# Performance work log

Hardware: AMD Instinct MI355X
Metric: run time of the kernel (lower is better)

The kernel has to match this reference:

```python
import jax, jax.numpy as jnp
import numpy as np

N = 100000
E = 1000000
IN_DIM = 64
ATT_DIM = 32


def setup_inputs() -> dict:
    key = jax.random.key(0)
    ks = jax.random.split(key, 9)
    x = jax.random.normal(ks[0], (N, IN_DIM), dtype=jnp.float32)
    src1 = jax.random.randint(ks[1], (E,), 0, N, dtype=jnp.int32)
    dst1 = jax.random.randint(ks[2], (E,), 0, N, dtype=jnp.int32)
    src2 = jax.random.randint(ks[3], (E,), 0, N, dtype=jnp.int32)
    dst2 = jax.random.randint(ks[4], (E,), 0, N, dtype=jnp.int32)
    # Learned params: w_o (in_dim -> att_dim), att (att_dim -> 1)
    W_o = jax.random.normal(ks[5], (IN_DIM, ATT_DIM), dtype=jnp.float32) / np.sqrt(IN_DIM)
    b_o = jnp.zeros((ATT_DIM,), dtype=jnp.float32)
    W_att = jax.random.normal(ks[6], (ATT_DIM, 1), dtype=jnp.float32) / np.sqrt(ATT_DIM)
    b_att = jnp.zeros((1,), dtype=jnp.float32)
    return {"x": x, "W_o": W_o, "b_o": b_o, "W_att": W_att, "b_att": b_att,
            "src1": src1, "dst1": dst1, "src2": src2, "dst2": dst2}


def _edge_softmax_agg(h, a, src, dst):
    """edge_softmax of source logits grouped by dst, then weighted sum of src feats."""
    a_e = a[src]  # [E] per-edge logit copied from source node (copy_u)
    m = jax.ops.segment_max(a_e, dst, num_segments=N)  # per-dst max for stability
    m = jnp.where(jnp.isfinite(m), m, 0.0)
    e = jnp.exp(a_e - jax.lax.stop_gradient(m)[dst])
    s = jax.ops.segment_sum(e, dst, num_segments=N)  # per-dst normalizer
    w = e / s[dst]  # normalized edge attention [E]
    # u_mul_e + sum reduction
    return jax.ops.segment_sum(h[src] * w[:, None], dst, num_segments=N)  # [N, in_dim]


def reference(x, W_o, b_o, W_att, b_att, src1, dst1, src2, dst2):
    # a = att(w_o(h))  (note: self.activation is defined but unused in forward)
    a = ((x @ W_o + b_o) @ W_att + b_att)[:, 0]  # [N]
    h1 = _edge_softmax_agg(x, a, src1, dst1)
    h2 = _edge_softmax_agg(x, a, src2, dst2)
    # multi_update_all cross-type 'mean' over the 2 edge types
    return (h1 + h2) * 0.5
```

## Files before the change

kernel.cpp:

```cpp
#include <hip/hip_runtime.h>
#include <hip/hip_bf16.h>

#define IN_DIM 64
#define BSHIFT 7
#define BSIZE  128
#define CHUNK  8192
#define PBLK   512
#define MAXNB1 1024
#define CAPMAX 1600
#define GBLK   256

__device__ __forceinline__ float bflo(unsigned int u) { return __uint_as_float(u << 16); }
__device__ __forceinline__ float bfhi(unsigned int u) { return __uint_as_float(u & 0xFFFF0000u); }
__device__ __forceinline__ unsigned short f2bf(float f) {
    __hip_bfloat16 b = __float2bfloat16(f);
    return *reinterpret_cast<unsigned short*>(&b);
}

#define ACC8(A, e, v)                        \
    A[0] = fmaf(e, bflo((v).x), A[0]);       \
    A[1] = fmaf(e, bfhi((v).x), A[1]);       \
    A[2] = fmaf(e, bflo((v).y), A[2]);       \
    A[3] = fmaf(e, bfhi((v).y), A[3]);       \
    A[4] = fmaf(e, bflo((v).z), A[4]);       \
    A[5] = fmaf(e, bfhi((v).z), A[5]);       \
    A[6] = fmaf(e, bflo((v).w), A[6]);       \
    A[7] = fmaf(e, bfhi((v).w), A[7]);

__global__ __launch_bounds__(PBLK) void logits_partition_kernel(
        const float* __restrict__ x,
        const float* __restrict__ W_o,
        const float* __restrict__ b_o,
        const float* __restrict__ W_att,
        const float* __restrict__ b_att,
        float* __restrict__ ea,
        unsigned short* __restrict__ xh, int N,
        const int* __restrict__ src1,
        const int* __restrict__ dst1,
        const int* __restrict__ src2,
        const int* __restrict__ dst2,
        int* __restrict__ gCtr,
        int* __restrict__ packed,
        int E, int NB1, int CAP, int chunks1) {
    __shared__ int spk[CHUNK];
    __shared__ unsigned short sbk[CHUNK];
    __shared__ int hist[MAXNB1];
    __shared__ int lbase[MAXNB1];
    __shared__ int gb2[MAXNB1];
    __shared__ int scr[PBLK];
    __shared__ float vsh[IN_DIM];
    __shared__ float csh;
    int pb = 2 * chunks1;
    int t = threadIdx.x;
    if (blockIdx.x < pb) {
        int b = blockIdx.x;
        int type = (b >= chunks1) ? 1 : 0;
        int ci = type ? (b - chunks1) : b;
        const int* src = type ? src2 : src1;
        const int* dst = type ? dst2 : dst1;
        int e0 = ci * CHUNK;
        int e1 = min(E, e0 + CHUNK);
        int cnt = e1 - e0;
        for (int i = t; i < MAXNB1; i += PBLK) hist[i] = 0;
        __syncthreads();
        for (int e = e0 + t; e < e1; e += PBLK)
            atomicAdd(&hist[dst[e] >> BSHIFT], 1);
        __syncthreads();
        int a0 = hist[2 * t], a1 = hist[2 * t + 1];
        int s = a0 + a1;
        scr[t] = s;
        __syncthreads();
        int val = s;
        for (int off = 1; off < PBLK; off <<= 1) {
            int u = (t >= off) ? scr[t - off] : 0;
            __syncthreads();
            val += u;
            scr[t] = val;
            __syncthreads();
        }
        int ex = val - s;
        lbase[2 * t] = ex;
        lbase[2 * t + 1] = ex + a0;
        __syncthreads();
        for (int i = t; i < NB1; i += PBLK) {
            int h = hist[i];
            gb2[i] = (h ? atomicAdd(&gCtr[type * NB1 + i], h) : 0) - lbase[i];
            hist[i] = lbase[i];
        }
        __syncthreads();
        for (int e = e0 + t; e < e1; e += PBLK) {
            int d = dst[e];
            int bk = d >> BSHIFT;
            int lrank = atomicAdd(&hist[bk], 1);
            spk[lrank] = src[e] | ((d & (BSIZE - 1)) << 17);
            sbk[lrank] = (unsigned short)bk;
        }
        __syncthreads();
        for (int i = t; i < cnt; i += PBLK) {
            int bk = sbk[i];
            int lrk = gb2[bk] + i;
            if (lrk < CAP)
                packed[(size_t)(type * NB1 + bk) * CAP + lrk] = spk[i];
        }
    } else {
        if (t < IN_DIM) {
            float acc = 0.f;
#pragma unroll
            for (int k = 0; k < 32; ++k) acc += W_o[t * 32 + k] * W_att[k];
            vsh[t] = acc;
        }
        if (t == IN_DIM) {
            float acc = b_att[0];
#pragma unroll
            for (int k = 0; k < 32; ++k) acc += b_o[k] * W_att[k];
            csh = acc;
        }
        __syncthreads();
        int node = (blockIdx.x - pb) * 32 + (t >> 4);
        int fq = t & 15;
        if (node >= N) return;
        const float4 xv = *(const float4*)(x + (size_t)node * 64 + fq * 4);
        ushort4 st;
        st.x = f2bf(xv.x); st.y = f2bf(xv.y); st.z = f2bf(xv.z); st.w = f2bf(xv.w);
        *(ushort4*)(xh + (size_t)node * 64 + fq * 4) = st;
        float val = xv.x * vsh[fq * 4 + 0] + xv.y * vsh[fq * 4 + 1] +
                    xv.z * vsh[fq * 4 + 2] + xv.w * vsh[fq * 4 + 3];
        val += __shfl_xor(val, 1);
        val += __shfl_xor(val, 2);
        val += __shfl_xor(val, 4);
        val += __shfl_xor(val, 8);
        if (fq == 0) ea[node] = expf(val + csh);
    }
}

__global__ __launch_bounds__(GBLK, 5) void csr_gather_kernel(
        const int* __restrict__ gCtr,
        const int* __restrict__ packed,
        const float* __restrict__ ea,
        const unsigned short* __restrict__ xh,
        float* __restrict__ out, int N, int NB1, int CAP) {
    __shared__ int2 pae[2][CAPMAX];
    __shared__ int  hist[2][BSIZE];
    __shared__ int  exv [2][BSIZE];
    __shared__ int  cur [BSIZE];
    int nb = blockIdx.x;
    int t = threadIdx.x;

#pragma unroll
    for (int type = 0; type < 2; ++type) {
        int r = type * NB1 + nb;
        int cnt = min(gCtr[r], CAP);
        const int* seg = packed + (size_t)r * CAP;
        if (t < BSIZE) hist[type][t] = 0;
        __syncthreads();
        for (int i = t; i < cnt; i += GBLK)
            atomicAdd(&hist[type][seg[i] >> 17], 1);
        __syncthreads();
        int v = 0, val = 0;
        if (t < BSIZE) { v = hist[type][t]; val = v; cur[t] = v; }
        __syncthreads();
        for (int off = 1; off < BSIZE; off <<= 1) {
            int u = 0;
            if (t < BSIZE && t >= off) u = cur[t - off];
            __syncthreads();
            if (t < BSIZE) { val += u; cur[t] = val; }
            __syncthreads();
        }
        if (t < BSIZE) { exv[type][t] = val - v; cur[t] = val - v; }
        __syncthreads();
        for (int i = t; i < cnt; i += GBLK) {
            int p = seg[i];
            int s = p & 0x1FFFF;
            int pos = atomicAdd(&cur[p >> 17], 1);
            pae[type][pos] = make_int2(s, __float_as_int(ea[s]));
        }
        __syncthreads();
    }

    int gid = t >> 3;
    int fl  = t & 7;
    const unsigned short* xrow = xh + (fl << 3);

    for (int ni = 0; ni < 4; ++ni) {
        int dl = (ni << 5) + gid;
        float rr[8] = {0,0,0,0,0,0,0,0};
#pragma unroll
        for (int type = 0; type < 2; ++type) {
            int k0 = exv[type][dl];
            int deg = hist[type][dl];
            if (deg <= 0) continue;
            float accP[8] = {0,0,0,0,0,0,0,0};
            float accQ[8] = {0,0,0,0,0,0,0,0};
            float ewP = 0.f, ewQ = 0.f;
            int h = deg >> 1;
            for (int j = 0; j < h; ++j) {
                int2 p1 = pae[type][k0 + j];
                int2 p2 = pae[type][k0 + h + j];
                const uint4 v1 = *(const uint4*)(xrow + (size_t)p1.x * 64);
                const uint4 v2 = *(const uint4*)(xrow + (size_t)p2.x * 64);
                float e1 = __int_as_float(p1.y);
                float e2 = __int_as_float(p2.y);
                ewP += e1; ewQ += e2;
                ACC8(accP, e1, v1);
                ACC8(accQ, e2, v2);
            }
            if (deg & 1) {
                int2 p1 = pae[type][k0 + deg - 1];
                const uint4 v1 = *(const uint4*)(xrow + (size_t)p1.x * 64);
                float e1 = __int_as_float(p1.y);
                ewP += e1;
                ACC8(accP, e1, v1);
            }
            float inv = 1.f / (ewP + ewQ);
#pragma unroll
            for (int k = 0; k < 8; ++k)
                rr[k] = fmaf(accP[k] + accQ[k], inv, rr[k]);
        }
        int node = (nb << BSHIFT) + dl;
        if (node < N) {
            float* op = out + (size_t)node * 64 + (fl << 3);
            *(float4*)op       = make_float4(0.5f * rr[0], 0.5f * rr[1], 0.5f * rr[2], 0.5f * rr[3]);
            *(float4*)(op + 4) = make_float4(0.5f * rr[4], 0.5f * rr[5], 0.5f * rr[6], 0.5f * rr[7]);
        }
    }
}

extern "C" void kernel_launch(void* const* d_in, const int* in_sizes, int n_in,
                              void* d_out, int out_size, void* d_ws, size_t ws_size,
                              hipStream_t stream) {
    const float* x     = (const float*)d_in[0];
    const float* W_o   = (const float*)d_in[1];
    const float* b_o   = (const float*)d_in[2];
    const float* W_att = (const float*)d_in[3];
    const float* b_att = (const float*)d_in[4];
    const int*   src1  = (const int*)d_in[5];
    const int*   dst1  = (const int*)d_in[6];
    const int*   src2  = (const int*)d_in[7];
    const int*   dst2  = (const int*)d_in[8];
    float* out = (float*)d_out;

    const int N = in_sizes[0] / IN_DIM;
    const int E = in_sizes[5];
    const int NB1 = (N + BSIZE - 1) >> BSHIFT;
    const int avg = (E + NB1 - 1) / NB1;
    int CAP = avg + avg / 6 + 32;
    if (CAP > CAPMAX) CAP = CAPMAX;

    char* wp = (char*)d_ws;
    auto take = [&](size_t bytes) { char* p = wp; wp += (bytes + 63) & ~63ull; return p; };
    float* ea          = (float*)take((size_t)N * 4);
    int* gCtr          = (int*)take((size_t)2 * NB1 * 4);
    unsigned short* xh = (unsigned short*)take((size_t)N * 64 * 2);
    int* packed        = (int*)take((size_t)2 * NB1 * CAP * 4);

    hipMemsetAsync(gCtr, 0, (size_t)2 * NB1 * sizeof(int), stream);

    int chunks1 = (E + CHUNK - 1) / CHUNK;
    int logitBlocks = (N + 31) / 32;
    logits_partition_kernel<<<2 * chunks1 + logitBlocks, PBLK, 0, stream>>>(
        x, W_o, b_o, W_att, b_att, ea, xh, N,
        src1, dst1, src2, dst2, gCtr, packed, E, NB1, CAP, chunks1);

    csr_gather_kernel<<<NB1, GBLK, 0, stream>>>(gCtr, packed, ea, xh, out,
                                                N, NB1, CAP);
}
```

Baseline: 80.60 us.

## Use wavefront shuffle scans and degree-sorted node assignment in gather

```diff
diff --git a/kernel.cpp b/kernel.cpp
--- a/kernel.cpp
+++ b/kernel.cpp
@@ -47,7 +47,7 @@
     __shared__ int hist[MAXNB1];
     __shared__ int lbase[MAXNB1];
     __shared__ int gb2[MAXNB1];
-    __shared__ int scr[PBLK];
+    __shared__ int wsum[8];
     __shared__ float vsh[IN_DIM];
     __shared__ float csh;
     int pb = 2 * chunks1;
@@ -68,17 +68,20 @@
         __syncthreads();
         int a0 = hist[2 * t], a1 = hist[2 * t + 1];
         int s = a0 + a1;
-        scr[t] = s;
-        __syncthreads();
+        int lane = t & 63;
+        int wv = t >> 6;
         int val = s;
-        for (int off = 1; off < PBLK; off <<= 1) {
-            int u = (t >= off) ? scr[t - off] : 0;
-            __syncthreads();
-            val += u;
-            scr[t] = val;
-            __syncthreads();
-        }
-        int ex = val - s;
+#pragma unroll
+        for (int off = 1; off < 64; off <<= 1) {
+            int u = __shfl_up(val, off);
+            if (lane >= off) val += u;
+        }
+        if (lane == 63) wsum[wv] = val;
+        __syncthreads();
+        int woff = 0;
+#pragma unroll
+        for (int w = 0; w < 7; ++w) woff += (w < wv) ? wsum[w] : 0;
+        int ex = val + woff - s;
         lbase[2 * t] = ex;
         lbase[2 * t + 1] = ex + a0;
         __syncthreads();
@@ -143,8 +146,12 @@
     __shared__ int  hist[2][BSIZE];
     __shared__ int  exv [2][BSIZE];
     __shared__ int  cur [BSIZE];
+    __shared__ int  nid [BSIZE];
+    __shared__ int  tdeg[BSIZE];
+    __shared__ int  w0sum;
     int nb = blockIdx.x;
     int t = threadIdx.x;
+    int lane = t & 63;
 
 #pragma unroll
     for (int type = 0; type < 2; ++type) {
@@ -156,16 +163,16 @@
         for (int i = t; i < cnt; i += GBLK)
             atomicAdd(&hist[type][seg[i] >> 17], 1);
         __syncthreads();
-        int v = 0, val = 0;
-        if (t < BSIZE) { v = hist[type][t]; val = v; cur[t] = v; }
-        __syncthreads();
-        for (int off = 1; off < BSIZE; off <<= 1) {
-            int u = 0;
-            if (t < BSIZE && t >= off) u = cur[t - off];
-            __syncthreads();
-            if (t < BSIZE) { val += u; cur[t] = val; }
-            __syncthreads();
-        }
+        int v = (t < BSIZE) ? hist[type][t] : 0;
+        int val = v;
+#pragma unroll
+        for (int off = 1; off < 64; off <<= 1) {
+            int u = __shfl_up(val, off);
+            if (lane >= off) val += u;
+        }
+        if (t == 63) w0sum = val;
+        __syncthreads();
+        if (t >= 64 && t < BSIZE) val += w0sum;
         if (t < BSIZE) { exv[type][t] = val - v; cur[t] = val - v; }
         __syncthreads();
         for (int i = t; i < cnt; i += GBLK) {
@@ -177,12 +184,25 @@
         __syncthreads();
     }
 
+    if (t < BSIZE) tdeg[t] = hist[0][t] + hist[1][t];
+    __syncthreads();
+    if (t < BSIZE) {
+        int td = tdeg[t];
+        int rank = 0;
+        for (int j = 0; j < BSIZE; ++j) {
+            int oj = tdeg[j];
+            rank += (oj > td) || (oj == td && j < t);
+        }
+        nid[rank] = t;
+    }
+    __syncthreads();
+
     int gid = t >> 3;
     int fl  = t & 7;
     const unsigned short* xrow = xh + (fl << 3);
 
     for (int ni = 0; ni < 4; ++ni) {
-        int dl = (ni << 5) + gid;
+        int dl = nid[(ni << 5) + gid];
         float rr[8] = {0,0,0,0,0,0,0,0};
 #pragma unroll
         for (int type = 0; type < 2; ++type) {
```

New measurement: 83.33 us. 3.4% more time.
